# Performance work log

Measured on AMD Instinct MI355X. Metric: run time of the kernel, lower is better.

Reference implementation:

```python
import jax, jax.numpy as jnp
import numpy as np
from jax import lax

CHAR_H = 100
HIDDEN = 512
N_LABELS = 64
WORD_D = 300
CHAR_D = 50
FORGET_BIAS = 1.0
BN_EPS = 1e-3


def lstm(x, W, b, lens):
    """TF BasicLSTMCell dynamic_rnn. x:[B,T,D], W:[D+H,4H], b:[4H], lens:[B].
    Returns (outputs [B,T,H] zeroed past lens, (c,h) final states held at lens)."""
    B, T, _ = x.shape
    H = W.shape[1] // 4
    def step(carry, inp):
        c, h = carry
        xt, t = inp
        z = jnp.concatenate([xt, h], axis=-1) @ W + b
        i, j, f, o = jnp.split(z, 4, axis=-1)  # TF gate order i, j(g), f, o
        c_new = c * jax.nn.sigmoid(f + FORGET_BIAS) + jax.nn.sigmoid(i) * jnp.tanh(j)
        h_new = jnp.tanh(c_new) * jax.nn.sigmoid(o)
        active = (t < lens)[:, None]
        c = jnp.where(active, c_new, c)
        h = jnp.where(active, h_new, h)
        out = jnp.where(active, h_new, jnp.zeros_like(h_new))
        return (c, h), out
    init = (jnp.zeros((B, H), x.dtype), jnp.zeros((B, H), x.dtype))
    (c, h), outs = lax.scan(step, init, (jnp.swapaxes(x, 0, 1), jnp.arange(T)))
    return jnp.swapaxes(outs, 0, 1), (c, h)


def reverse_seq(x, lens):
    """tf.reverse_sequence along time axis 1."""
    T = x.shape[1]
    t = jnp.arange(T)[None, :]
    idx = jnp.where(t < lens[:, None], lens[:, None] - 1 - t, t)
    return jnp.take_along_axis(x, idx[:, :, None], axis=1)


def _glorot(key, shape):
    fan_in, fan_out = shape[0], shape[1]
    s = np.sqrt(6.0 / (fan_in + fan_out)).astype(np.float32)
    return jax.random.uniform(key, shape, jnp.float32, -s, s)


def setup_inputs() -> dict:
    key = jax.random.key(0)
    ks = jax.random.split(key, 16)
    N_SUB, SUB_T = 16384, 25
    B, T = 64, 256
    d_word_in = WORD_D + 2 * CHAR_H  # 500
    inp = {
        "subwords": jax.random.normal(ks[0], (N_SUB, SUB_T, CHAR_D), jnp.float32),
        "tokens": jax.random.normal(ks[1], (B, T, WORD_D), jnp.float32),
        "token_subword": jax.random.randint(ks[2], (B, T), 0, N_SUB, jnp.int32),
        "subword_seq_lens": jax.random.randint(ks[3], (N_SUB,), 1, SUB_T + 1, jnp.int32),
        "seq_lens": jax.random.randint(ks[4], (B,), 1, T + 1, jnp.int32),
        "Wc_f": _glorot(ks[5], (CHAR_D + CHAR_H, 4 * CHAR_H)),
        "bc_f": jnp.zeros((4 * CHAR_H,), jnp.float32),
        "Wc_b": _glorot(ks[6], (CHAR_D + CHAR_H, 4 * CHAR_H)),
        "bc_b": jnp.zeros((4 * CHAR_H,), jnp.float32),
        "Ww_f": _glorot(ks[7], (d_word_in + HIDDEN, 4 * HIDDEN)),
        "bw_f": jnp.zeros((4 * HIDDEN,), jnp.float32),
        "Ww_b": _glorot(ks[8], (d_word_in + HIDDEN, 4 * HIDDEN)),
        "bw_b": jnp.zeros((4 * HIDDEN,), jnp.float32),
        "Wo": _glorot(ks[9], (2 * HIDDEN + HIDDEN, 4 * HIDDEN)),
        "bo": jnp.zeros((4 * HIDDEN,), jnp.float32),
        "bn_gamma": jnp.ones((HIDDEN,), jnp.float32),
        "bn_beta": jnp.zeros((HIDDEN,), jnp.float32),
        "Wt": _glorot(ks[10], (HIDDEN, N_LABELS)),
        "bt": jnp.zeros((N_LABELS,), jnp.float32),
    }
    return inp


def reference(subwords, tokens, token_subword, subword_seq_lens, seq_lens,
              Wc_f, bc_f, Wc_b, bc_b, Ww_f, bw_f, Ww_b, bw_b,
              Wo, bo, bn_gamma, bn_beta, Wt, bt):
    # --- char/subword BiLSTM: only final hidden states are used ---
    _, (_, hf) = lstm(subwords, Wc_f, bc_f, subword_seq_lens)
    _, (_, hb) = lstm(reverse_seq(subwords, subword_seq_lens), Wc_b, bc_b, subword_seq_lens)
    subword_reprs = jnp.concatenate([hf, hb], axis=1)           # [N_sub, 200]
    tok_sub = subword_reprs[token_subword]                      # [B,T,200]
    word_in = jnp.concatenate([tokens, tok_sub], axis=2)        # [B,T,500]
    # --- word BiLSTM ---
    f_out, _ = lstm(word_in, Ww_f, bw_f, seq_lens)
    b_out_r, _ = lstm(reverse_seq(word_in, seq_lens), Ww_b, bw_b, seq_lens)
    b_out = reverse_seq(b_out_r, seq_lens)
    hidden = jnp.concatenate([f_out, b_out], axis=2)            # [B,T,1024]
    # --- top unidirectional LSTM ---
    out2, _ = lstm(hidden, Wo, bo, seq_lens)                    # [B,T,512]
    # --- batch norm over all but last dim (contrib.layers.batch_norm) ---
    mean = jnp.mean(out2, axis=(0, 1))
    var = jnp.var(out2, axis=(0, 1))
    bn = bn_gamma * (out2 - mean) * lax.rsqrt(var + BN_EPS) + bn_beta
    # --- tag affine ---
    logits = bn @ Wt + bt                                       # [B,T,n_labels]
    return logits
```

## Files before the change

### kernel.cpp

```cpp
#include <hip/hip_runtime.h>
#include <cstdint>
#include <cstddef>


typedef unsigned short bf_t;
typedef __attribute__((ext_vector_type(8))) short bf16x8;
typedef __attribute__((ext_vector_type(4))) float f32x4;

#define DEVI __device__ __forceinline__
DEVI float bf2f(bf_t u){ return __uint_as_float(((unsigned)u)<<16); }
DEVI bf_t  f2bf(float f){ unsigned u=__float_as_uint(f); return (bf_t)((u + 0x7FFFu + ((u>>16)&1u))>>16); }
DEVI float sigx(float x){ return __builtin_amdgcn_rcpf(1.0f + __builtin_amdgcn_exp2f(-1.44269504f*x)); }
DEVI float tanx(float x){ return 2.0f*__builtin_amdgcn_rcpf(1.0f + __builtin_amdgcn_exp2f(-2.88539008f*x)) - 1.0f; }

__global__ void k_dbg(float* out, unsigned mb){ out[0] = (float)mb; }

__global__ __launch_bounds__(256) void k_prep_charm(const float* __restrict__ wcf,
    const float* __restrict__ wcb, bf_t* __restrict__ wct){
  int i = blockIdx.x*256 + threadIdx.x;
  if (i >= 2*400*160) return;
  int kk = i % 160; int r = i / 160;
  int np = r % 400; int dir = r / 400;
  int u = np >> 2, g = np & 3;
  const float* w = dir ? wcb : wcf;
  wct[i] = (kk < 150) ? f2bf(w[kk*400 + g*100 + u]) : (bf_t)0;
}
__global__ __launch_bounds__(256) void k_prep_wrec(const float* __restrict__ wwf,
    const float* __restrict__ wwb, bf_t* __restrict__ wrg){
  int i = blockIdx.x*256 + threadIdx.x;
  if (i >= 2*2048*512) return;
  int k = i & 511; int np = (i >> 9) & 2047; int dir = i >> 20;
  int c = np >> 2, g = np & 3;
  const float* w = dir ? wwb : wwf;
  wrg[i] = f2bf(w[(size_t)(500 + k)*2048 + g*512 + c]);
}
__global__ __launch_bounds__(256) void k_prep_trec(const float* __restrict__ wo,
    bf_t* __restrict__ wog){
  int i = blockIdx.x*256 + threadIdx.x;
  if (i >= 2048*512) return;
  int k = i & 511; int np = i >> 9;
  int c = np >> 2, g = np & 3;
  wog[i] = f2bf(wo[(size_t)(1024 + k)*2048 + g*512 + c]);
}
__global__ __launch_bounds__(256) void k_prep_wx(const float* __restrict__ wwf,
    const float* __restrict__ wwb, bf_t* __restrict__ wx){
  int i = blockIdx.x*256 + threadIdx.x;
  if (i >= 2*2048*512) return;
  int k = i & 511; int r = i >> 9;
  int np = r & 2047; int dir = r >> 11;
  int c = np >> 2, g = np & 3;
  const float* w = dir ? wwb : wwf;
  wx[i] = (k < 500) ? f2bf(w[(size_t)k*2048 + g*512 + c]) : (bf_t)0;
}
__global__ __launch_bounds__(256) void k_prep_wxt(const float* __restrict__ wo,
    bf_t* __restrict__ wxt){
  int i = blockIdx.x*256 + threadIdx.x;
  if (i >= 2048*1024) return;
  int k = i & 1023; int np = i >> 10;
  int c = np >> 2, g = np & 3;
  wxt[i] = f2bf(wo[(size_t)k*2048 + g*512 + c]);
}
__global__ __launch_bounds__(256) void k_prep_bias(const float* __restrict__ bwf,
    const float* __restrict__ bwb, const float* __restrict__ bo,
    float* __restrict__ bpf, float* __restrict__ bpb, float* __restrict__ bpt){
  int np = blockIdx.x*256 + threadIdx.x;
  if (np >= 2048) return;
  int c = np >> 2, g = np & 3;
  bpf[np] = bwf[g*512 + c];
  bpb[np] = bwb[g*512 + c];
  bpt[np] = bo[g*512 + c];
}
__global__ __launch_bounds__(256) void k_ridx(const int* __restrict__ lens,
    int* __restrict__ ridxb){
  int b = blockIdx.x, t = threadIdx.x;
  int L = lens[b];
  int tin = (t < L) ? (L - 1 - t) : t;
  ridxb[b*256 + t] = b*256 + tin;
}

DEVI int aslot(int s, int kk){
  return (((kk >> 5)*4 + ((kk >> 3) & 3))*16 + s)*8 + (kk & 7);
}
__global__ __launch_bounds__(256) void k_charm(const float* __restrict__ subwords,
    const int* __restrict__ slens, const bf_t* __restrict__ wct,
    const float* __restrict__ bcf, const float* __restrict__ bcb,
    bf_t* __restrict__ rep){
  const int dir = blockIdx.y;
  const int s0 = blockIdx.x * 16;
  const int tid = threadIdx.x;
  const int w = tid >> 6, lane = tid & 63;
  const int l16 = lane & 15, lk = lane >> 4;

  __shared__ __align__(16) bf_t abuf[2560];
  __shared__ float zs[16][409];
  __shared__ float bs[400];
  __shared__ int lens[16];

  if (tid < 16) lens[tid] = slens[s0 + tid];
  for (int i = tid; i < 1280; i += 256) ((float*)abuf)[i] = 0.f;
  {
    const float* bc = dir ? bcb : bcf;
    for (int i = tid; i < 400; i += 256) bs[i] = bc[(i & 3)*100 + (i >> 2)];
  }
  __syncthreads();

  const bf_t* wctd = wct + (size_t)dir*400*160;
  float c7[7];
#pragma unroll
  for (int j = 0; j < 7; j++) c7[j] = 0.f;

  for (int t = 0; t < 25; t++) {
    for (int i = tid; i < 800; i += 256) {
      int s = i / 50, k = i - s*50;
      int L = lens[s];
      int te = dir ? (L - 1 - t) : t;
      te = te < 0 ? 0 : te;
      abuf[aslot(s, k)] = f2bf(subwords[((size_t)(s0 + s)*25 + te)*50 + k]);
    }
    __syncthreads();

    f32x4 acc[7];
#pragma unroll
    for (int jj = 0; jj < 7; jj++) acc[jj] = (f32x4){0.f,0.f,0.f,0.f};
#pragma unroll
    for (int ks = 0; ks < 5; ks++) {
      bf16x8 af = *(const bf16x8*)&abuf[((ks*4 + lk)*16 + l16)*8];
#pragma unroll
      for (int jj = 0; jj < 7; jj++) {
        int j = w + jj*4;
        if (j < 25) {
          bf16x8 bv = *(const bf16x8*)(wctd + (size_t)(j*16 + l16)*160 + ks*32 + lk*8);
          acc[jj] = __builtin_amdgcn_mfma_f32_16x16x32_bf16(af, bv, acc[jj], 0, 0, 0);
        }
      }
    }
#pragma unroll
    for (int jj = 0; jj < 7; jj++) {
      int j = w + jj*4;
      if (j < 25) {
#pragma unroll
        for (int r = 0; r < 4; r++)
          zs[lk*4 + r][j*16 + l16] = acc[jj][r];
      }
    }
    __syncthreads();

#pragma unroll
    for (int j = 0; j < 7; j++) {
      int idx = j*256 + tid;
      if (idx < 1600) {
        int s = idx & 15, u = idx >> 4;
        int L = lens[s];
        if (t < L) {
          float zi = zs[s][u*4 + 0] + bs[u*4 + 0];
          float zj = zs[s][u*4 + 1] + bs[u*4 + 1];
          float zf = zs[s][u*4 + 2] + bs[u*4 + 2];
          float zo = zs[s][u*4 + 3] + bs[u*4 + 3];
          float cn = c7[j]*sigx(zf + 1.0f) + sigx(zi)*tanx(zj);
          float hn = tanx(cn)*sigx(zo);
          c7[j] = cn;
          bf_t hb = f2bf(hn);
          abuf[aslot(s, 50 + u)] = hb;
          if (t == L - 1) rep[(size_t)(s0 + s)*200 + dir*100 + u] = hb;
        }
      }
    }
  }
}

__global__ __launch_bounds__(128) void k_win(const float* __restrict__ tokens,
    const bf_t* __restrict__ rep, const int* __restrict__ tsub,
    bf_t* __restrict__ win){
  int row = blockIdx.x;
  int idx = tsub[row];
  const float* tsrc = tokens + (size_t)row*300;
  const bf_t* rsrc = rep + (size_t)idx*200;
  bf_t* w = win + (size_t)row*512;
  for (int i = threadIdx.x; i < 512; i += 128)
    w[i] = (i < 300) ? f2bf(tsrc[i]) : (i < 500 ? rsrc[i - 300] : (bf_t)0);
}

__global__ __launch_bounds__(256) void k_mgemm(const bf_t* __restrict__ A, int lda, int K,
    const bf_t* __restrict__ B0, const bf_t* __restrict__ B1,
    const float* __restrict__ bp0, const float* __restrict__ bp1,
    bf_t* __restrict__ C0, bf_t* __restrict__ C1,
    const int* __restrict__ ridx1, int t0){
  const int z = blockIdx.z;
  const bf_t* B = z ? B1 : B0;
  const float* bp = z ? bp1 : bp0;
  bf_t* C = z ? C1 : C0;
  const int* ridx = z ? ridx1 : nullptr;
  __shared__ short As[4096];
  __shared__ short Bs[4096];
  const int tid = threadIdx.x;
  const int rb = blockIdx.y*128, nb = blockIdx.x*128;
  const bf_t* srcA[2]; const bf_t* srcB[2];
#pragma unroll
  for (int q = 0; q < 2; q++) {
    int s = tid + q*256;
    int row = ((s >> 6) << 4) + (s & 15), kg = (s >> 4) & 3;
    int lr = rb + row;
    int v = (t0 >= 0) ? ((lr >> 6)*256 + t0 + (lr & 63)) : lr;
    int ga = ridx ? ridx[v] : v;
    srcA[q] = A + (size_t)ga*lda + kg*8;
    srcB[q] = B + (size_t)(nb + row)*K + kg*8;
  }
  f32x4 acc[4][4];
#pragma unroll
  for (int i = 0; i < 4; i++)
#pragma unroll
    for (int j = 0; j < 4; j++) acc[i][j] = (f32x4){0.f,0.f,0.f,0.f};
  const int wid = tid >> 6, lane = tid & 63;
  const int wr = wid >> 1, wc = wid & 1;
  const int l16 = lane & 15, lk = lane >> 4;

  uint4 va0 = *(const uint4*)(srcA[0]);
  uint4 va1 = *(const uint4*)(srcA[1]);
  uint4 vb0 = *(const uint4*)(srcB[0]);
  uint4 vb1 = *(const uint4*)(srcB[1]);
  for (int kb = 0; kb < K; kb += 32) {
    __syncthreads();
    *(uint4*)&As[(size_t)tid*8] = va0;
    *(uint4*)&As[(size_t)(tid+256)*8] = va1;
    *(uint4*)&Bs[(size_t)tid*8] = vb0;
    *(uint4*)&Bs[(size_t)(tid+256)*8] = vb1;
    __syncthreads();
    if (kb + 32 < K) {
      va0 = *(const uint4*)(srcA[0] + kb + 32);
      va1 = *(const uint4*)(srcA[1] + kb + 32);
      vb0 = *(const uint4*)(srcB[0] + kb + 32);
      vb1 = *(const uint4*)(srcB[1] + kb + 32);
    }
    bf16x8 af[4], bfr[4];
#pragma unroll
    for (int f = 0; f < 4; f++) {
      af[f]  = *(const bf16x8*)&As[(((wr*4 + f)*4 + lk)*16 + l16)*8];
      bfr[f] = *(const bf16x8*)&Bs[(((wc*4 + f)*4 + lk)*16 + l16)*8];
    }
#pragma unroll
    for (int i = 0; i < 4; i++)
#pragma unroll
      for (int j = 0; j < 4; j++)
        acc[i][j] = __builtin_amdgcn_mfma_f32_16x16x32_bf16(af[i], bfr[j], acc[i][j], 0, 0, 0);
  }
#pragma unroll
  for (int i = 0; i < 4; i++) {
    int row0 = wr*64 + i*16 + lk*4;
#pragma unroll
    for (int j = 0; j < 4; j++) {
      int col = nb + wc*64 + j*16 + l16;
      float bv = bp[col];
#pragma unroll
      for (int r = 0; r < 4; r++)
        C[(size_t)(rb + row0 + r)*2048 + col] = f2bf(acc[i][j][r] + bv);
    }
  }
}

__global__ __launch_bounds__(512) void k_chunk(
    bf_t* __restrict__ hx0, bf_t* __restrict__ hx1,
    float* __restrict__ cst, const bf_t* __restrict__ wrec,
    const bf_t* __restrict__ zxf, const bf_t* __restrict__ zxb,
    const int* __restrict__ seq_lens, bf_t* __restrict__ outp,
    unsigned* __restrict__ ctrs, int t0, int is_top){
  const int dir = is_top ? 0 : blockIdx.y;
  const int n = blockIdx.x;
  const int npb = n*128;
  const unsigned nblk = gridDim.x;
  unsigned* ctr = ctrs + dir*32;
  const int tid = threadIdx.x;
  const int w = tid >> 6, lane = tid & 63;
  const int l16 = lane & 15, lk = lane >> 4;

  __shared__ __align__(16) char smem[65536];
  float (*zs)[132] = (float(*)[132])smem;

  const bf_t* B = wrec + ((size_t)dir*2048 + npb + w*16)*512;
  const bf_t* zx = (dir ? zxb : zxf);
  unsigned long long* hx08 = (unsigned long long*)hx0 + (size_t)dir*8192;
  unsigned long long* hx18 = (unsigned long long*)hx1 + (size_t)dir*8192;

  bf16x8 bfr[16];
#pragma unroll
  for (int ks = 0; ks < 16; ks++)
    bfr[ks] = *(const bf16x8*)(B + (size_t)l16*512 + ks*32 + lk*8);

  const int b = tid >> 3, q = tid & 7, u0 = q*4;
  const int len = seq_lens[b];
  const int cg0 = (npb >> 2) + u0;
  const size_t cbase = ((size_t)dir*64 + b)*512 + cg0;
  float creg[4];
#pragma unroll
  for (int it = 0; it < 4; it++) creg[it] = cst[cbase + it];
  const size_t hslot = (size_t)n*512 + b*8 + q;
  unsigned long long hpack = __hip_atomic_load(
      ((t0 & 1) ? hx18 : hx08) + hslot,
      __ATOMIC_RELAXED, __HIP_MEMORY_SCOPE_AGENT);

  for (int s = 0; s < 64; s++) {
    const int t = t0 + s;
    unsigned long long* hr8 = (t & 1) ? hx18 : hx08;
    unsigned long long* hw8 = (t & 1) ? hx08 : hx18;

    const int tl = t & 63;
    uint4 zq[2];
    {
      const char* zxp = (const char*)(zx + ((size_t)(b*64 + tl))*2048 + (size_t)(npb + u0*4));
      zq[0] = *(const uint4*)zxp;
      zq[1] = *(const uint4*)(zxp + 16);
    }

#pragma unroll
    for (int it = 0; it < 16; it++) {
      int i = it*512 + tid;
      int nn = i >> 9, r9 = i & 511;
      int bb = r9 >> 3, qq = r9 & 7;
      unsigned long long v = __hip_atomic_load(hr8 + i,
          __ATOMIC_RELAXED, __HIP_MEMORY_SCOPE_AGENT);
      int cb = nn*64 + qq*8;
      *(unsigned long long*)&smem[bb*1024 + (((cb & ~15) ^ ((bb & 7) << 4)) | (cb & 15))] = v;
    }
    __syncthreads();

    f32x4 acc[4];
#pragma unroll
    for (int mf = 0; mf < 4; mf++) acc[mf] = (f32x4){0.f,0.f,0.f,0.f};
#pragma unroll
    for (int ks = 0; ks < 16; ks++) {
#pragma unroll
      for (int mf = 0; mf < 4; mf++) {
        int row = mf*16 + l16;
        bf16x8 af = *(const bf16x8*)&smem[row*1024 + ((ks*64 + lk*16) ^ ((row & 7) << 4))];
        acc[mf] = __builtin_amdgcn_mfma_f32_16x16x32_bf16(af, bfr[ks], acc[mf], 0, 0, 0);
      }
    }
    __syncthreads();

#pragma unroll
    for (int mf = 0; mf < 4; mf++)
#pragma unroll
      for (int r = 0; r < 4; r++)
        zs[mf*16 + lk*4 + r][w*16 + l16] = acc[mf][r];
    __syncthreads();

    if (t < len) {
      const ushort* zu = (const ushort*)zq;
      bf_t hb4[4];
#pragma unroll
      for (int it = 0; it < 4; it++) {
        float zi = zs[b][(u0 + it)*4 + 0] + bf2f(zu[it*4 + 0]);
        float zj = zs[b][(u0 + it)*4 + 1] + bf2f(zu[it*4 + 1]);
        float zf = zs[b][(u0 + it)*4 + 2] + bf2f(zu[it*4 + 2]);
        float zo = zs[b][(u0 + it)*4 + 3] + bf2f(zu[it*4 + 3]);
        float cn = creg[it]*sigx(zf + 1.0f) + sigx(zi)*tanx(zj);
        float hn = tanx(cn)*sigx(zo);
        creg[it] = cn;
        hb4[it] = f2bf(hn);
      }
      hpack = *(unsigned long long*)hb4;
      if (is_top) {
        *(ushort4*)&outp[((size_t)b*256 + t)*512 + cg0] = *(ushort4*)hb4;
      } else {
        int tin = dir ? (len - 1 - t) : t;
        *(ushort4*)&outp[((size_t)b*256 + tin)*1024 + dir*512 + cg0] = *(ushort4*)hb4;
      }
    }
    __hip_atomic_store(hw8 + hslot, hpack,
                       __ATOMIC_RELAXED, __HIP_MEMORY_SCOPE_AGENT);

    __syncthreads();
    if (tid == 0) {
      __hip_atomic_fetch_add(ctr, 1u, __ATOMIC_RELAXED, __HIP_MEMORY_SCOPE_AGENT);
      unsigned tgt = (unsigned)(s + 1) * nblk;
      while (__hip_atomic_load(ctr, __ATOMIC_RELAXED, __HIP_MEMORY_SCOPE_AGENT) < tgt) {
        __builtin_amdgcn_s_sleep(1);
      }
    }
    __syncthreads();
  }
#pragma unroll
  for (int it = 0; it < 4; it++) cst[cbase + it] = creg[it];
}

__global__ __launch_bounds__(256) void k_gemm_tag(const bf_t* __restrict__ A, int lda, int K,
    const float* __restrict__ W, int ldw, const float* __restrict__ bias,
    float* __restrict__ C, int ldc){
  const int nb = blockIdx.x*64, rb = blockIdx.y*128;
  const int tid = threadIdx.x;
  const int tr = tid >> 4, tc = tid & 15;
  __shared__ float As[16][132];
  __shared__ float Bs[16][68];
  float acc[8][4];
#pragma unroll
  for (int i = 0; i < 8; i++)
#pragma unroll
    for (int j = 0; j < 4; j++) acc[i][j] = 0.f;
  const int ar = tid >> 1, ak = (tid & 1)*8;
  const int bk = tid >> 4, bn = (tid & 15)*4;
  const bf_t* arow = A + (size_t)(rb + ar)*lda;
  for (int kb = 0; kb < K; kb += 16) {
#pragma unroll
    for (int j = 0; j < 8; j++)
      As[ak + j][ar] = bf2f(arow[kb + ak + j]);
    const float* wp = W + (size_t)(kb + bk)*ldw + nb + bn;
    Bs[bk][bn] = wp[0]; Bs[bk][bn+1] = wp[1]; Bs[bk][bn+2] = wp[2]; Bs[bk][bn+3] = wp[3];
    __syncthreads();
#pragma unroll
    for (int kk = 0; kk < 16; kk++) {
      float4 a0 = *(const float4*)&As[kk][tr*8];
      float4 a1 = *(const float4*)&As[kk][tr*8 + 4];
      float4 bq = *(const float4*)&Bs[kk][tc*4];
      float av[8] = {a0.x,a0.y,a0.z,a0.w,a1.x,a1.y,a1.z,a1.w};
      float bv[4] = {bq.x,bq.y,bq.z,bq.w};
#pragma unroll
      for (int i = 0; i < 8; i++)
#pragma unroll
        for (int j = 0; j < 4; j++) acc[i][j] += av[i]*bv[j];
    }
    __syncthreads();
  }
  float4 bb = *(const float4*)&bias[nb + tc*4];
  float bias4[4] = {bb.x, bb.y, bb.z, bb.w};
#pragma unroll
  for (int i = 0; i < 8; i++) {
    size_t row = rb + tr*8 + i;
#pragma unroll
    for (int j = 0; j < 4; j++)
      C[row*(size_t)ldc + nb + tc*4 + j] = acc[i][j] + bias4[j];
  }
}

__global__ __launch_bounds__(512) void k_bnstats(const bf_t* __restrict__ out2,
    float* __restrict__ gsum, float* __restrict__ gsq){
  int c = threadIdx.x;
  int r0 = blockIdx.x*256;
  float s = 0.f, q = 0.f;
  for (int i = 0; i < 256; i++) {
    float v = bf2f(out2[(size_t)(r0 + i)*512 + c]);
    s += v; q += v*v;
  }
  atomicAdd(&gsum[c], s);
  atomicAdd(&gsq[c], q);
}

__global__ __launch_bounds__(512) void k_bnfin(const float* __restrict__ gsum,
    const float* __restrict__ gsq, const float* __restrict__ gamma,
    const float* __restrict__ beta, const float* __restrict__ wt,
    const float* __restrict__ bt, float* __restrict__ wtp, float* __restrict__ btp){
  __shared__ float a_s[512], d_s[512];
  int c = threadIdx.x;
  float mean = gsum[c] * (1.0f/16384.0f);
  float var  = gsq[c]  * (1.0f/16384.0f) - mean*mean;
  float a = gamma[c] * rsqrtf(var + 1e-3f);
  a_s[c] = a;
  d_s[c] = beta[c] - mean*a;
  __syncthreads();
  for (int i = c; i < 512*64; i += 512) wtp[i] = a_s[i >> 6] * wt[i];
  if (c < 64) {
    float acc = bt[c];
    for (int cc = 0; cc < 512; cc++) acc += d_s[cc] * wt[cc*64 + c];
    btp[c] = acc;
  }
}

extern "C" void kernel_launch(void* const* d_in, const int* in_sizes, int n_in,
                              void* d_out, int out_size, void* d_ws, size_t ws_size,
                              hipStream_t stream) {
  const float* subwords = (const float*)d_in[0];
  const float* tokens   = (const float*)d_in[1];
  const int*   tsub     = (const int*)d_in[2];
  const int*   sublens  = (const int*)d_in[3];
  const int*   seqlens  = (const int*)d_in[4];
  const float* wcf = (const float*)d_in[5];
  const float* bcf = (const float*)d_in[6];
  const float* wcb = (const float*)d_in[7];
  const float* bcb = (const float*)d_in[8];
  const float* wwf = (const float*)d_in[9];
  const float* bwf = (const float*)d_in[10];
  const float* wwb = (const float*)d_in[11];
  const float* bwb = (const float*)d_in[12];
  const float* wo  = (const float*)d_in[13];
  const float* bo  = (const float*)d_in[14];
  const float* gma = (const float*)d_in[15];
  const float* bta = (const float*)d_in[16];
  const float* wt  = (const float*)d_in[17];
  const float* btb = (const float*)d_in[18];
  float* out = (float*)d_out;

  char* ws = (char*)d_ws;
  size_t off = 0;
  auto alc = [&](size_t bytes) -> void* {
    void* p = ws + off;
    off += (bytes + 255) & ~(size_t)255;
    return p;
  };
  bf_t* REP   = (bf_t*)alc(16384ull*200*2);
  bf_t* WIN   = (bf_t*)alc(16384ull*512*2);
  int*  RIDXB = (int*) alc(16384ull*4);
  bf_t* ZXF   = (bf_t*)alc(4096ull*2048*2);
  bf_t* ZXB   = (bf_t*)alc(4096ull*2048*2);
  bf_t* HID   = (bf_t*)alc(16384ull*1024*2);
  const size_t STATB = 131072 + 131072 + 65536 + 65536 + 262144 + 131072
                     + 2048 + 2048 + 2048;
  char* STAT0 = (char*)alc(STATB);
  bf_t* HXW0 = (bf_t*)STAT0;
  bf_t* HXW1 = (bf_t*)(STAT0 + 131072);
  bf_t* HXT0 = (bf_t*)(STAT0 + 262144);
  bf_t* HXT1 = (bf_t*)(STAT0 + 327680);
  float* CSW = (float*)(STAT0 + 393216);
  float* CST = (float*)(STAT0 + 655360);
  float* GSUM = (float*)(STAT0 + 786432);
  float* GSQ  = (float*)(STAT0 + 788480);
  unsigned* CTRS = (unsigned*)(STAT0 + 790528);
  float* WTP  = (float*)alc(512ull*64*4);
  float* BTP  = (float*)alc(64*4);
  bf_t* WCT  = (bf_t*)alc(2ull*400*160*2);
  bf_t* WRG  = (bf_t*)alc(2ull*2048*512*2);
  bf_t* WOG  = (bf_t*)alc(2048ull*512*2);
  bf_t* WXG  = (bf_t*)alc(2ull*2048*512*2);
  bf_t* WXT  = (bf_t*)alc(2048ull*1024*2);
  float* BPF = (float*)alc(2048*4);
  float* BPB = (float*)alc(2048*4);
  float* BPT = (float*)alc(2048*4);
  bf_t* ZXT  = ZXF;
  bf_t* OUT2 = ZXB;
  if (off > ws_size) {
    k_dbg<<<1, 1, 0, stream>>>(out, (unsigned)(ws_size >> 20));
    return;
  }

  hipMemsetAsync(HID, 0, 16384ull*1024*2, stream);
  hipMemsetAsync(STAT0, 0, STATB, stream);

  k_prep_charm<<<500, 256, 0, stream>>>(wcf, wcb, WCT);
  k_prep_wrec<<<8192, 256, 0, stream>>>(wwf, wwb, WRG);
  k_prep_trec<<<4096, 256, 0, stream>>>(wo, WOG);
  k_prep_wx<<<8192, 256, 0, stream>>>(wwf, wwb, WXG);
  k_prep_wxt<<<8192, 256, 0, stream>>>(wo, WXT);
  k_prep_bias<<<8, 256, 0, stream>>>(bwf, bwb, bo, BPF, BPB, BPT);
  k_ridx<<<64, 256, 0, stream>>>(seqlens, RIDXB);

  k_charm<<<dim3(1024, 2), 256, 0, stream>>>(subwords, sublens, WCT, bcf, bcb, REP);
  k_win<<<16384, 128, 0, stream>>>(tokens, REP, tsub, WIN);

  for (int ch = 0; ch < 4; ch++) {
    k_mgemm<<<dim3(16, 32, 2), 256, 0, stream>>>(WIN, 512, 512,
        WXG, WXG + 2048ull*512, BPF, BPB, ZXF, ZXB, RIDXB, ch*64);
    k_chunk<<<dim3(16, 2), 512, 0, stream>>>(HXW0, HXW1, CSW, WRG, ZXF, ZXB,
                                             seqlens, HID, CTRS + ch*64, ch*64, 0);
  }

  hipMemsetAsync(OUT2, 0, 16384ull*512*2, stream);
  for (int ch = 0; ch < 4; ch++) {
    k_mgemm<<<dim3(16, 32, 1), 256, 0, stream>>>(HID, 1024, 1024,
        WXT, nullptr, BPT, nullptr, ZXT, nullptr, nullptr, ch*64);
    k_chunk<<<dim3(16, 1), 512, 0, stream>>>(HXT0, HXT1, CST, WOG, ZXT, nullptr,
                                             seqlens, OUT2, CTRS + 256 + ch*32, ch*64, 1);
  }

  k_bnstats<<<64, 512, 0, stream>>>(OUT2, GSUM, GSQ);
  k_bnfin<<<1, 512, 0, stream>>>(GSUM, GSQ, gma, bta, wt, btb, WTP, BTP);
  k_gemm_tag<<<dim3(1, 128, 1), 256, 0, stream>>>(OUT2, 512, 512, WTP, 64, BTP, out, 64);
}
```

Baseline: 5.079 ms.

## Swap MFMA operands in recurrent step and prefetch char-LSTM inputs

```diff
diff --git a/kernel.cpp b/kernel.cpp
--- a/kernel.cpp
+++ b/kernel.cpp
@@ -104,20 +104,39 @@
   }
   __syncthreads();
 
+  int si[4], ki[4], Lr[4]; bool vr[4];
+#pragma unroll
+  for (int r = 0; r < 4; r++) {
+    int i = tid + r*256;
+    vr[r] = (i < 800);
+    si[r] = vr[r] ? (i / 50) : 0;
+    ki[r] = vr[r] ? (i - si[r]*50) : 0;
+    Lr[r] = lens[si[r]];
+  }
+  float pf[4];
+  auto loadx = [&](int t){
+#pragma unroll
+    for (int r = 0; r < 4; r++) {
+      if (vr[r]) {
+        int te = dir ? (Lr[r] - 1 - t) : t;
+        te = te < 0 ? 0 : te;
+        pf[r] = subwords[((size_t)(s0 + si[r])*25 + te)*50 + ki[r]];
+      }
+    }
+  };
+  loadx(0);
+
   const bf_t* wctd = wct + (size_t)dir*400*160;
   float c7[7];
 #pragma unroll
   for (int j = 0; j < 7; j++) c7[j] = 0.f;
 
   for (int t = 0; t < 25; t++) {
-    for (int i = tid; i < 800; i += 256) {
-      int s = i / 50, k = i - s*50;
-      int L = lens[s];
-      int te = dir ? (L - 1 - t) : t;
-      te = te < 0 ? 0 : te;
-      abuf[aslot(s, k)] = f2bf(subwords[((size_t)(s0 + s)*25 + te)*50 + k]);
-    }
-    __syncthreads();
+#pragma unroll
+    for (int r = 0; r < 4; r++)
+      if (vr[r]) abuf[aslot(si[r], ki[r])] = f2bf(pf[r]);
+    __syncthreads();
+    if (t < 24) loadx(t + 1);
 
     f32x4 acc[7];
 #pragma unroll
@@ -273,29 +292,33 @@
   const int l16 = lane & 15, lk = lane >> 4;
 
   __shared__ __align__(16) char smem[65536];
-  float (*zs)[132] = (float(*)[132])smem;
+  bf_t* hsh = (bf_t*)smem;
 
   const bf_t* B = wrec + ((size_t)dir*2048 + npb + w*16)*512;
   const bf_t* zx = (dir ? zxb : zxf);
   unsigned long long* hx08 = (unsigned long long*)hx0 + (size_t)dir*8192;
   unsigned long long* hx18 = (unsigned long long*)hx1 + (size_t)dir*8192;
-
-  bf16x8 bfr[16];
+  bf_t* hxh0 = (bf_t*)hx0 + (size_t)dir*65536/2;
+  bf_t* hxh1 = (bf_t*)hx1 + (size_t)dir*65536/2;
+
+  bf16x8 wfr[16];
 #pragma unroll
   for (int ks = 0; ks < 16; ks++)
-    bfr[ks] = *(const bf16x8*)(B + (size_t)l16*512 + ks*32 + lk*8);
-
-  const int b = tid >> 3, q = tid & 7, u0 = q*4;
-  const int len = seq_lens[b];
-  const int cg0 = (npb >> 2) + u0;
-  const size_t cbase = ((size_t)dir*64 + b)*512 + cg0;
-  float creg[4];
-#pragma unroll
-  for (int it = 0; it < 4; it++) creg[it] = cst[cbase + it];
-  const size_t hslot = (size_t)n*512 + b*8 + q;
-  unsigned long long hpack = __hip_atomic_load(
-      ((t0 & 1) ? hx18 : hx08) + hslot,
-      __ATOMIC_RELAXED, __HIP_MEMORY_SCOPE_AGENT);
+    wfr[ks] = *(const bf16x8*)(B + (size_t)l16*512 + ks*32 + lk*8);
+
+  const int c_local = w*4 + lk;
+  const int cg = (npb >> 2) + c_local;
+  int len4[4]; float creg[4]; bf_t hreg[4];
+  {
+    const bf_t* hinit = (t0 & 1) ? hxh1 : hxh0;
+#pragma unroll
+    for (int bt = 0; bt < 4; bt++) {
+      int b = bt*16 + l16;
+      len4[bt] = seq_lens[b];
+      creg[bt] = cst[((size_t)dir*64 + b)*512 + cg];
+      hreg[bt] = hinit[n*2048 + b*32 + c_local];
+    }
+  }
 
   for (int s = 0; s < 64; s++) {
     const int t = t0 + s;
@@ -303,11 +326,11 @@
     unsigned long long* hw8 = (t & 1) ? hx08 : hx18;
 
     const int tl = t & 63;
-    uint4 zq[2];
-    {
-      const char* zxp = (const char*)(zx + ((size_t)(b*64 + tl))*2048 + (size_t)(npb + u0*4));
-      zq[0] = *(const uint4*)zxp;
-      zq[1] = *(const uint4*)(zxp + 16);
+    ushort4 zq4[4];
+#pragma unroll
+    for (int bt = 0; bt < 4; bt++) {
+      int b = bt*16 + l16;
+      zq4[bt] = *(const ushort4*)(zx + ((size_t)(b*64 + tl))*2048 + npb + w*16 + lk*4);
     }
 
 #pragma unroll
@@ -324,49 +347,48 @@
 
     f32x4 acc[4];
 #pragma unroll
-    for (int mf = 0; mf < 4; mf++) acc[mf] = (f32x4){0.f,0.f,0.f,0.f};
+    for (int bt = 0; bt < 4; bt++) acc[bt] = (f32x4){0.f,0.f,0.f,0.f};
 #pragma unroll
     for (int ks = 0; ks < 16; ks++) {
 #pragma unroll
-      for (int mf = 0; mf < 4; mf++) {
-        int row = mf*16 + l16;
-        bf16x8 af = *(const bf16x8*)&smem[row*1024 + ((ks*64 + lk*16) ^ ((row & 7) << 4))];
-        acc[mf] = __builtin_amdgcn_mfma_f32_16x16x32_bf16(af, bfr[ks], acc[mf], 0, 0, 0);
-      }
-    }
-    __syncthreads();
-
-#pragma unroll
-    for (int mf = 0; mf < 4; mf++)
-#pragma unroll
-      for (int r = 0; r < 4; r++)
-        zs[mf*16 + lk*4 + r][w*16 + l16] = acc[mf][r];
-    __syncthreads();
-
-    if (t < len) {
-      const ushort* zu = (const ushort*)zq;
-      bf_t hb4[4];
-#pragma unroll
-      for (int it = 0; it < 4; it++) {
-        float zi = zs[b][(u0 + it)*4 + 0] + bf2f(zu[it*4 + 0]);
-        float zj = zs[b][(u0 + it)*4 + 1] + bf2f(zu[it*4 + 1]);
-        float zf = zs[b][(u0 + it)*4 + 2] + bf2f(zu[it*4 + 2]);
-        float zo = zs[b][(u0 + it)*4 + 3] + bf2f(zu[it*4 + 3]);
-        float cn = creg[it]*sigx(zf + 1.0f) + sigx(zi)*tanx(zj);
+      for (int bt = 0; bt < 4; bt++) {
+        int row = bt*16 + l16;
+        bf16x8 hf = *(const bf16x8*)&smem[row*1024 + ((ks*64 + lk*16) ^ ((row & 7) << 4))];
+        acc[bt] = __builtin_amdgcn_mfma_f32_16x16x32_bf16(wfr[ks], hf, acc[bt], 0, 0, 0);
+      }
+    }
+    __syncthreads();
+
+#pragma unroll
+    for (int bt = 0; bt < 4; bt++) {
+      int b = bt*16 + l16;
+      int len = len4[bt];
+      if (t < len) {
+        float zi = acc[bt][0] + bf2f(zq4[bt].x);
+        float zj = acc[bt][1] + bf2f(zq4[bt].y);
+        float zf = acc[bt][2] + bf2f(zq4[bt].z);
+        float zo = acc[bt][3] + bf2f(zq4[bt].w);
+        float cn = creg[bt]*sigx(zf + 1.0f) + sigx(zi)*tanx(zj);
         float hn = tanx(cn)*sigx(zo);
-        creg[it] = cn;
-        hb4[it] = f2bf(hn);
-      }
-      hpack = *(unsigned long long*)hb4;
-      if (is_top) {
-        *(ushort4*)&outp[((size_t)b*256 + t)*512 + cg0] = *(ushort4*)hb4;
-      } else {
-        int tin = dir ? (len - 1 - t) : t;
-        *(ushort4*)&outp[((size_t)b*256 + tin)*1024 + dir*512 + cg0] = *(ushort4*)hb4;
-      }
-    }
-    __hip_atomic_store(hw8 + hslot, hpack,
-                       __ATOMIC_RELAXED, __HIP_MEMORY_SCOPE_AGENT);
+        creg[bt] = cn;
+        hreg[bt] = f2bf(hn);
+        if (is_top) {
+          outp[((size_t)b*256 + t)*512 + cg] = hreg[bt];
+        } else {
+          int tin = dir ? (len - 1 - t) : t;
+          outp[((size_t)b*256 + tin)*1024 + dir*512 + cg] = hreg[bt];
+        }
+      }
+      hsh[b*40 + c_local] = hreg[bt];
+    }
+    __syncthreads();
+
+    {
+      int pb = tid >> 3, pq = tid & 7;
+      unsigned long long pv = *(const unsigned long long*)&hsh[pb*40 + pq*4];
+      __hip_atomic_store(hw8 + (size_t)n*512 + pb*8 + pq, pv,
+                         __ATOMIC_RELAXED, __HIP_MEMORY_SCOPE_AGENT);
+    }
 
     __syncthreads();
     if (tid == 0) {
@@ -379,7 +401,8 @@
     __syncthreads();
   }
 #pragma unroll
-  for (int it = 0; it < 4; it++) cst[cbase + it] = creg[it];
+  for (int bt = 0; bt < 4; bt++)
+    cst[((size_t)dir*64 + bt*16 + l16)*512 + cg] = creg[bt];
 }
 
 __global__ __launch_bounds__(256) void k_gemm_tag(const bf_t* __restrict__ A, int lda, int K,
```

Result: slower. 5.418 ms (+6.7%).
